# Optimization experiments

Measured on AMD Instinct MI355X. Metric: run time of the kernel, lower is better.

The kernel has to match this reference:

```python
import jax, jax.numpy as jnp
import numpy as np

S, B, N, A, L = 2, 8, 12, 4, 24
C, AUX, EK, K, M, OTH = 256, 16, 64, 256, 8, 32
D2 = C + AUX          # transfromer2 d_model
FF = 2048             # torch TransformerEncoderLayer default dim_feedforward
RIN = 2 * EK + 2 * D2 + 2 * OTH
NLAYERS = 2


def _layernorm(x, g, b, eps=1e-5):
    mu = x.mean(-1, keepdims=True)
    var = ((x - mu) ** 2).mean(-1, keepdims=True)
    return (x - mu) * jax.lax.rsqrt(var + eps) * g + b


def _mha(x, Wq, bq, Wk, bk, Wv, bv, Wo, bo):
    # x: [seq, batch, d]; single head (nhead=1), torch seq-first semantics
    q = x @ Wq.T + bq
    k = x @ Wk.T + bk
    v = x @ Wv.T + bv
    scale = x.shape[-1] ** -0.5
    att = jax.nn.softmax(jnp.einsum('sbd,tbd->bst', q, k) * scale, axis=-1)
    o = jnp.einsum('bst,tbd->sbd', att, v)
    return o @ Wo.T + bo


def _encoder(x, aw, ab, w1, b1, w2, b2, lg, lb):
    # post-norm torch TransformerEncoderLayer, ReLU FFN, dropout off (eval)
    for i in range(aw.shape[0]):
        a = _mha(x, aw[i, 0], ab[i, 0], aw[i, 1], ab[i, 1], aw[i, 2], ab[i, 2], aw[i, 3], ab[i, 3])
        x = _layernorm(x + a, lg[i, 0], lb[i, 0])
        h = jax.nn.relu(x @ w1[i].T + b1[i]) @ w2[i].T + b2[i]
        x = _layernorm(x + h, lg[i, 1], lb[i, 1])
    return x


def _conv(x, w, b, pad):
    y = jax.lax.conv_general_dilated(x, w, (1, 1), [(pad, pad), (0, 0)],
                                     dimension_numbers=('NCHW', 'OIHW', 'NCHW'))
    return y + b[None, :, None, None]


def _forward(chars, att_type, kw_idx, input_idx, static, other,
             char_table, filter_w, filter_b, gate_w, gate_b, mlp_w, mlp_b,
             kw_table, aline_w, aline_b,
             t1_attn_w, t1_attn_b, t1_ffn_w1, t1_ffn_b1, t1_ffn_w2, t1_ffn_b2, t1_ln_g, t1_ln_b,
             t2_attn_w, t2_attn_b, t2_ffn_w1, t2_ffn_b1, t2_ffn_w2, t2_ffn_b2, t2_ln_g, t2_ln_b,
             reg_w1, reg_b1, reg_w2, reg_b2):
    # nn.Embedding(max_norm=1): rows renormalized to norm <= 1
    nrm = jnp.linalg.norm(char_table, axis=1, keepdims=True)
    tbl = char_table * jnp.minimum(1.0, 1.0 / jnp.maximum(nrm, 1e-7))
    ce = tbl[chars]                                  # [S,B,N,A,L,C]
    x = ce.reshape(-1, 1, L, C)                      # strings as conv batch
    f = jnp.tanh(_conv(x, filter_w, filter_b, 1))    # gated conv: tanh * sigmoid
    g = jax.nn.sigmoid(_conv(x, gate_w, gate_b, 1))
    v = _conv(f * g, mlp_w, mlp_b, 0)                # 1x1 conv back to 1 channel
    str_vec = v.reshape(S, B, N, A, L, C).mean(axis=4)   # mean over chars -> [S,B,N,A,C]
    kw_vec = kw_table[kw_idx] @ aline_w.T + aline_b      # keyword path -> [S,B,N,A,C]
    att_vec = jnp.where((att_type == 1)[..., None], kw_vec, str_vec)
    # transfromer1: torch seq-first, seq = nodes, batch = (side, plan, attr)
    x1 = att_vec.transpose(2, 0, 1, 3, 4).reshape(N, S * B * A, C)
    y1 = _encoder(x1, t1_attn_w, t1_attn_b, t1_ffn_w1, t1_ffn_b1, t1_ffn_w2, t1_ffn_b2, t1_ln_g, t1_ln_b)
    node_enc = y1.reshape(N, S, B, A, C).mean(axis=3).transpose(1, 2, 0, 3)  # mean over attrs -> [S,B,N,C]
    h = jnp.concatenate([node_enc, static], axis=-1)                          # [S,B,N,D2]
    # transfromer2: seq = plan batch, batch = (side, node) -- torch seq-first
    x2 = h.transpose(1, 0, 2, 3).reshape(B, S * N, D2)
    y2 = _encoder(x2, t2_attn_w, t2_attn_b, t2_ffn_w1, t2_ffn_b1, t2_ffn_w2, t2_ffn_b2, t2_ln_g, t2_ln_b)
    real = y2.reshape(B, S, N, D2).mean(axis=2)      # mean over nodes -> [B,S,D2]
    inp = kw_table[input_idx].mean(axis=2)           # encoding_input -> [S,B,EK]
    feats = jnp.concatenate([inp[0], real[:, 0], inp[1], real[:, 1], other], axis=1)  # [B,RIN]
    return jax.nn.relu(feats @ reg_w1.T + reg_b1) @ reg_w2.T + reg_b2  # [B,1]


def setup_inputs() -> dict:
    key = jax.random.key(0)
    ks = iter(jax.random.split(key, 64))
    def rn(shape, s=0.02):
        return jax.random.normal(next(ks), shape, jnp.float32) * s
    inp = {
        'chars': jax.random.randint(next(ks), (S, B, N, A, L), 0, 128, jnp.int32),
        'att_type': jax.random.randint(next(ks), (S, B, N, A), 0, 2, jnp.int32),
        'kw_idx': jax.random.randint(next(ks), (S, B, N, A), 0, K, jnp.int32),
        'input_idx': jax.random.randint(next(ks), (S, B, M), 0, K, jnp.int32),
        'static': rn((S, B, N, AUX), 1.0),
        'other': rn((B, 2 * OTH), 1.0),
        'char_table': rn((128, C), 1.0),
        'filter_w': rn((16, 1, 3, 1), 0.2), 'filter_b': rn((16,), 0.02),
        'gate_w': rn((16, 1, 3, 1), 0.2), 'gate_b': rn((16,), 0.02),
        'mlp_w': rn((1, 16, 1, 1), 0.2), 'mlp_b': rn((1,), 0.02),
        'kw_table': rn((K, EK), 0.05),
        'aline_w': rn((C, EK), 0.05), 'aline_b': rn((C,), 0.02),
        't1_attn_w': rn((NLAYERS, 4, C, C), 0.05), 't1_attn_b': rn((NLAYERS, 4, C), 0.02),
        't1_ffn_w1': rn((NLAYERS, FF, C), 0.02), 't1_ffn_b1': rn((NLAYERS, FF), 0.02),
        't1_ffn_w2': rn((NLAYERS, C, FF), 0.02), 't1_ffn_b2': rn((NLAYERS, C), 0.02),
        't1_ln_g': jnp.ones((NLAYERS, 2, C), jnp.float32), 't1_ln_b': jnp.zeros((NLAYERS, 2, C), jnp.float32),
        't2_attn_w': rn((NLAYERS, 4, D2, D2), 0.05), 't2_attn_b': rn((NLAYERS, 4, D2), 0.02),
        't2_ffn_w1': rn((NLAYERS, FF, D2), 0.02), 't2_ffn_b1': rn((NLAYERS, FF), 0.02),
        't2_ffn_w2': rn((NLAYERS, D2, FF), 0.02), 't2_ffn_b2': rn((NLAYERS, D2), 0.02),
        't2_ln_g': jnp.ones((NLAYERS, 2, D2), jnp.float32), 't2_ln_b': jnp.zeros((NLAYERS, 2, D2), jnp.float32),
        'reg_w1': rn((32, RIN), 0.05), 'reg_b1': rn((32,), 0.02),
        'reg_w2': rn((1, 32), 0.1), 'reg_b2': rn((1,), 0.02),
    }
    return inp


def reference(chars, att_type, kw_idx, input_idx, static, other,
              char_table, filter_w, filter_b, gate_w, gate_b, mlp_w, mlp_b,
              kw_table, aline_w, aline_b,
              t1_attn_w, t1_attn_b, t1_ffn_w1, t1_ffn_b1, t1_ffn_w2, t1_ffn_b2, t1_ln_g, t1_ln_b,
              t2_attn_w, t2_attn_b, t2_ffn_w1, t2_ffn_b1, t2_ffn_w2, t2_ffn_b2, t2_ln_g, t2_ln_b,
              reg_w1, reg_b1, reg_w2, reg_b2):
    return _forward(chars, att_type, kw_idx, input_idx, static, other,
                    char_table, filter_w, filter_b, gate_w, gate_b, mlp_w, mlp_b,
                    kw_table, aline_w, aline_b,
                    t1_attn_w, t1_attn_b, t1_ffn_w1, t1_ffn_b1, t1_ffn_w2, t1_ffn_b2, t1_ln_g, t1_ln_b,
                    t2_attn_w, t2_attn_b, t2_ffn_w1, t2_ffn_b1, t2_ffn_w2, t2_ffn_b2, t2_ln_g, t2_ln_b,
                    reg_w1, reg_b1, reg_w2, reg_b2)
```

## Files before the change

kernel.cpp:

```cpp
#include <hip/hip_runtime.h>
#include <math.h>

#define S_ 2
#define B_ 8
#define N_ 12
#define A_ 4
#define L_ 24
#define C_ 256
#define AUX_ 16
#define EK_ 64
#define K_ 256
#define M_ 8
#define OTH_ 32
#define D2_ 272
#define FF_ 2048
#define RIN_ 736
#define NSTR_ (S_*B_*N_*A_)

typedef __attribute__((ext_vector_type(8))) short short8v;
typedef __attribute__((ext_vector_type(4))) float f32x4;

__device__ __forceinline__ unsigned short f2bf(float f) {
    unsigned u = __float_as_uint(f);
    return (unsigned short)((u + 0x7FFFu + ((u >> 16) & 1u)) >> 16);
}

__global__ void cvt_w_k(const float* __restrict__ s0, const float* __restrict__ s1,
                        const float* __restrict__ s2, const float* __restrict__ s3,
                        const float* __restrict__ s4, const float* __restrict__ s5,
                        unsigned short* __restrict__ dst) {
    const int T = 5441536 / 4;
    for (int q = blockIdx.x * 256 + threadIdx.x; q < T; q += gridDim.x * 256) {
        int idx = q * 4;
        const float* src; int off;
        if      (idx < 524288)  { src = s0; off = 0; }
        else if (idx < 1572864) { src = s1; off = 524288; }
        else if (idx < 2621440) { src = s2; off = 1572864; }
        else if (idx < 3213312) { src = s3; off = 2621440; }
        else if (idx < 4327424) { src = s4; off = 3213312; }
        else                    { src = s5; off = 4327424; }
        float4 v = *(const float4*)(src + (idx - off));
        ushort4 o;
        o.x = f2bf(v.x); o.y = f2bf(v.y); o.z = f2bf(v.z); o.w = f2bf(v.w);
        *(ushort4*)(dst + idx) = o;
    }
}

__global__ void scale_table_k(const float* __restrict__ tbl, float* __restrict__ out) {
    int r = blockIdx.x;
    int c = threadIdx.x;
    float v = tbl[r * C_ + c];
    float sq = v * v;
    for (int off = 32; off; off >>= 1) sq += __shfl_down(sq, off);
    __shared__ float red[4];
    __shared__ float scl;
    if ((c & 63) == 0) red[c >> 6] = sq;
    __syncthreads();
    if (c == 0) {
        float n = sqrtf(red[0] + red[1] + red[2] + red[3]);
        scl = fminf(1.f, 1.f / fmaxf(n, 1e-7f));
    }
    __syncthreads();
    out[r * C_ + c] = v * scl;
}

__global__ void attvec_k(const int* __restrict__ chars, const int* __restrict__ att_type,
                         const int* __restrict__ kw_idx, const float* __restrict__ tblS,
                         const float* __restrict__ fw, const float* __restrict__ fb,
                         const float* __restrict__ gw, const float* __restrict__ gb,
                         const float* __restrict__ mw, const float* __restrict__ mb,
                         const float* __restrict__ kwt, const float* __restrict__ aw,
                         const float* __restrict__ ab, float* __restrict__ x1,
                         unsigned short* __restrict__ x1b) {
    int str = blockIdx.x;
    int tid = threadIdx.x;
    int grp = tid >> 8;
    int c = tid & 255;
    __shared__ int ch[L_];
    __shared__ float xv[L_ + 2][C_];
    __shared__ float part[4][C_];
    if (tid < L_) ch[tid] = chars[str * L_ + tid];
    __syncthreads();

    bool kw = (att_type[str] == 1);
    float partial;
    if (kw) {
        const float* kr = kwt + kw_idx[str] * EK_ + grp * 16;
        const float* awr = aw + c * EK_ + grp * 16;
        float acc = (grp == 0) ? ab[c] : 0.f;
        #pragma unroll
        for (int e = 0; e < 16; ++e) acc = fmaf(kr[e], awr[e], acc);
        partial = acc;
    } else {
        #pragma unroll
        for (int i = 0; i < 6; ++i) {
            int l = grp * 6 + i;
            xv[l + 1][c] = tblS[ch[l] * C_ + c];
        }
        if (grp == 0) xv[0][c] = 0.f;
        if (grp == 3) xv[L_ + 1][c] = 0.f;
        __syncthreads();

        float f0[4], f1[4], f2[4], fbv[4], g0[4], g1[4], g2[4], gbv[4], mwv[4];
        #pragma unroll
        for (int oo = 0; oo < 4; ++oo) {
            int o = grp * 4 + oo;
            f0[oo] = 2.f*fw[o*3]; f1[oo] = 2.f*fw[o*3+1]; f2[oo] = 2.f*fw[o*3+2];
            fbv[oo] = 2.f*fb[o];
            g0[oo] = gw[o*3]; g1[oo] = gw[o*3+1]; g2[oo] = gw[o*3+2];
            gbv[oo] = gb[o];
            mwv[oo] = mw[o];
        }
        float osum[4] = {0.f, 0.f, 0.f, 0.f};
        float xm = xv[0][c], x0 = xv[1][c];
        for (int l = 1; l <= L_; ++l) {
            float xp = xv[l + 1][c];
            #pragma unroll
            for (int oo = 0; oo < 4; ++oo) {
                float pf2 = fbv[oo] + f0[oo]*xm + f1[oo]*x0 + f2[oo]*xp;
                float pg  = gbv[oo] + g0[oo]*xm + g1[oo]*x0 + g2[oo]*xp;
                pf2 = fminf(fmaxf(pf2, -30.f), 30.f);
                pg  = fminf(fmaxf(pg,  -15.f), 15.f);
                float e1 = __expf(pf2);
                float e2 = __expf(pg);
                float num = (e1 - 1.f) * e2;
                float den = (e1 + 1.f) * (e2 + 1.f);
                osum[oo] = fmaf(num, __builtin_amdgcn_rcpf(den), osum[oo]);
            }
            xm = x0; x0 = xp;
        }
        partial = mwv[0]*osum[0] + mwv[1]*osum[1] + mwv[2]*osum[2] + mwv[3]*osum[3];
    }
    part[grp][c] = partial;
    __syncthreads();
    if (grp == 0) {
        int a = str & 3;
        int n = (str >> 2) % N_;
        int sb = str / (N_ * A_);
        int row = n * 64 + sb * 4 + a;
        float tot = part[0][c] + part[1][c] + part[2][c] + part[3][c];
        float out = kw ? tot : (mb[0] + tot * (1.f / 24.f));
        x1[row * C_ + c] = out;
        x1b[row * C_ + c] = f2bf(out);
    }
}

__global__ void gemm_mfma_k(const unsigned short* __restrict__ Ab,
                            const unsigned short* __restrict__ Wb,
                            const float* __restrict__ bias, float* __restrict__ Cf,
                            unsigned short* __restrict__ Cb,
                            int R, int K, int N, int relu, int kslice, int obf) {
    int tid = threadIdx.x;
    int wave = tid >> 6, lane = tid & 63;
    int fr = lane & 15, fq = lane >> 4;
    int m0 = blockIdx.y * 64;
    int n0 = blockIdx.x * 64 + wave * 16;
    int kbeg = blockIdx.z * kslice;
    int kend = min(kbeg + kslice, K);
    int col = n0 + fr;
    bool bok = col < N;
    const unsigned short* Wrow = Wb + (size_t)col * K;
    const unsigned short* Ar0 = Ab + (size_t)(m0 + fr) * K;
    const unsigned short* Ar1 = Ab + (size_t)(m0 + 16 + fr) * K;
    const unsigned short* Ar2 = Ab + (size_t)(m0 + 32 + fr) * K;
    const unsigned short* Ar3 = Ab + (size_t)(m0 + 48 + fr) * K;

    f32x4 acc0 = {0.f,0.f,0.f,0.f}, acc1 = {0.f,0.f,0.f,0.f};
    f32x4 acc2 = {0.f,0.f,0.f,0.f}, acc3 = {0.f,0.f,0.f,0.f};
    const short8v z8 = {0,0,0,0,0,0,0,0};

    for (int kt = kbeg; kt < kend; kt += 32) {
        int kl = kt + fq * 8;
        bool kv = (kl + 8 <= kend);
        short8v bf  = (bok && kv) ? *(const short8v*)(Wrow + kl) : z8;
        short8v af0 = kv ? *(const short8v*)(Ar0 + kl) : z8;
        short8v af1 = kv ? *(const short8v*)(Ar1 + kl) : z8;
        short8v af2 = kv ? *(const short8v*)(Ar2 + kl) : z8;
        short8v af3 = kv ? *(const short8v*)(Ar3 + kl) : z8;
        acc0 = __builtin_amdgcn_mfma_f32_16x16x32_bf16(af0, bf, acc0, 0, 0, 0);
        acc1 = __builtin_amdgcn_mfma_f32_16x16x32_bf16(af1, bf, acc1, 0, 0, 0);
        acc2 = __builtin_amdgcn_mfma_f32_16x16x32_bf16(af2, bf, acc2, 0, 0, 0);
        acc3 = __builtin_amdgcn_mfma_f32_16x16x32_bf16(af3, bf, acc3, 0, 0, 0);
    }

    if (!bok) return;
    bool direct = (gridDim.z == 1);
    float bv = direct ? bias[col] : 0.f;
    float* outf = direct ? Cf : (Cf + (size_t)blockIdx.z * R * N);
#define STOREACC(accv, mi) do {                                           \
        _Pragma("unroll")                                                 \
        for (int j = 0; j < 4; ++j) {                                     \
            int row = m0 + (mi)*16 + fq * 4 + j;                          \
            float v = accv[j] + bv;                                       \
            if (direct && relu) v = fmaxf(v, 0.f);                        \
            if (obf) Cb[(size_t)row * N + col] = f2bf(v);                 \
            else     outf[(size_t)row * N + col] = v;                     \
        }                                                                 \
    } while (0)
    STOREACC(acc0, 0); STOREACC(acc1, 1); STOREACC(acc2, 2); STOREACC(acc3, 3);
#undef STOREACC
}

__global__ void attn_k(const float* __restrict__ qkv, unsigned short* __restrict__ ob,
                       int seq, int batch, int d, float scale) {
    __shared__ float sm[3 * 12 * 256];
    __shared__ float sc[12 * 12];
    int j = blockIdx.x, tid = threadIdx.x;
    int sd = seq * d, s3 = 3 * d;
    float* qs = sm;
    float* ks = sm + sd;
    float* vs = sm + 2 * sd;
    for (int idx = tid; idx < sd; idx += 256) {
        int s = idx / d, c = idx - s * d;
        const float* base = qkv + (size_t)(s * batch + j) * s3 + c;
        qs[idx] = base[0];
        ks[idx] = base[d];
        vs[idx] = base[2 * d];
    }
    __syncthreads();
    for (int p = tid; p < seq * seq; p += 256) {
        int s = p / seq, t = p - s * seq;
        float acc = 0.f;
        const float* qp = qs + s * d;
        const float* kp = ks + t * d;
        for (int c = 0; c < d; ++c) acc += qp[c] * kp[c];
        sc[p] = acc * scale;
    }
    __syncthreads();
    if (tid < seq) {
        float m = -1e30f;
        for (int t = 0; t < seq; ++t) m = fmaxf(m, sc[tid * seq + t]);
        float ssum = 0.f;
        for (int t = 0; t < seq; ++t) {
            float e = __expf(sc[tid * seq + t] - m);
            sc[tid * seq + t] = e;
            ssum += e;
        }
        float inv = 1.f / ssum;
        for (int t = 0; t < seq; ++t) sc[tid * seq + t] *= inv;
    }
    __syncthreads();
    for (int c = tid; c < d; c += 256) {
        for (int s = 0; s < seq; ++s) {
            float acc = 0.f;
            for (int t = 0; t < seq; ++t) acc += sc[s * seq + t] * vs[t * d + c];
            ob[(size_t)(s * batch + j) * d + c] = f2bf(acc);
        }
    }
}

__global__ void redln_k(const float* __restrict__ part, const float* __restrict__ bias,
                        float* __restrict__ x, unsigned short* __restrict__ xb,
                        const float* __restrict__ g, const float* __restrict__ b,
                        int d, int NS, int RN) {
    int r = blockIdx.x, tid = threadIdx.x;
    __shared__ float red[10];
    const float* xr = x + (size_t)r * d;
    int i0 = tid, i1 = tid + 256;
    bool h0 = i0 < d, h1 = i1 < d;
    float v0 = 0.f, v1 = 0.f;
    if (h0) {
        v0 = xr[i0] + bias[i0];
        for (int z = 0; z < NS; ++z) v0 += part[(size_t)z * RN + (size_t)r * d + i0];
    }
    if (h1) {
        v1 = xr[i1] + bias[i1];
        for (int z = 0; z < NS; ++z) v1 += part[(size_t)z * RN + (size_t)r * d + i1];
    }
    float s = v0 + v1, ss = v0 * v0 + v1 * v1;
    for (int off = 32; off; off >>= 1) {
        s += __shfl_down(s, off);
        ss += __shfl_down(ss, off);
    }
    if ((tid & 63) == 0) { red[(tid >> 6) * 2] = s; red[(tid >> 6) * 2 + 1] = ss; }
    __syncthreads();
    if (tid == 0) {
        float S = red[0] + red[2] + red[4] + red[6];
        float SS = red[1] + red[3] + red[5] + red[7];
        float mu = S / d;
        float var = SS / d - mu * mu;
        red[8] = mu;
        red[9] = rsqrtf(var + 1e-5f);
    }
    __syncthreads();
    float mu = red[8], inv = red[9];
    float* xw = x + (size_t)r * d;
    if (h0) {
        float o = (v0 - mu) * inv * g[i0] + b[i0];
        xw[i0] = o; xb[(size_t)r * d + i0] = f2bf(o);
    }
    if (h1) {
        float o = (v1 - mu) * inv * g[i1] + b[i1];
        xw[i1] = o; xb[(size_t)r * d + i1] = f2bf(o);
    }
}

__global__ void build_x2_k(const float* __restrict__ y1, const float* __restrict__ stat,
                           float* __restrict__ x2, unsigned short* __restrict__ x2b) {
    int id = blockIdx.x;
    int n = id % N_;
    int b = (id / N_) % B_;
    int s = id / (N_ * B_);
    int orow = b * (S_ * N_) + s * N_ + n;
    for (int c = threadIdx.x; c < D2_; c += 256) {
        float v;
        if (c < C_) {
            int j0 = (s * B_ + b) * A_;
            float acc = 0.f;
            for (int a = 0; a < A_; ++a) acc += y1[(size_t)(n * 64 + j0 + a) * C_ + c];
            v = acc * 0.25f;
        } else {
            v = stat[((size_t)(s * B_ + b) * N_ + n) * AUX_ + (c - C_)];
        }
        x2[(size_t)orow * D2_ + c] = v;
        x2b[(size_t)orow * D2_ + c] = f2bf(v);
    }
}

__global__ void build_real_k(const float* __restrict__ y2, float* __restrict__ real) {
    int id = blockIdx.x;
    int s = id & 1, b = id >> 1;
    for (int c = threadIdx.x; c < D2_; c += 256) {
        float acc = 0.f;
        for (int n = 0; n < N_; ++n) acc += y2[(size_t)(b * 24 + s * N_ + n) * D2_ + c];
        real[(size_t)(b * 2 + s) * D2_ + c] = acc * (1.f / 12.f);
    }
}

__global__ void regressor_k(const float* __restrict__ real, const int* __restrict__ input_idx,
                            const float* __restrict__ kwt, const float* __restrict__ other,
                            const float* __restrict__ w1, const float* __restrict__ b1,
                            const float* __restrict__ w2, const float* __restrict__ b2,
                            float* __restrict__ out) {
    int b = blockIdx.x;
    int tid = threadIdx.x;
    __shared__ float feats[RIN_];
    __shared__ float hh[32];
    for (int i = tid; i < RIN_; i += 256) {
        float v;
        if (i < 64) {
            float acc = 0.f;
            for (int m = 0; m < M_; ++m) acc += kwt[input_idx[b * M_ + m] * EK_ + i];
            v = acc * 0.125f;
        } else if (i < 336) {
            v = real[(size_t)(b * 2 + 0) * D2_ + (i - 64)];
        } else if (i < 400) {
            int e = i - 336;
            float acc = 0.f;
            for (int m = 0; m < M_; ++m) acc += kwt[input_idx[64 + b * M_ + m] * EK_ + e];
            v = acc * 0.125f;
        } else if (i < 672) {
            v = real[(size_t)(b * 2 + 1) * D2_ + (i - 400)];
        } else {
            v = other[b * 64 + (i - 672)];
        }
        feats[i] = v;
    }
    __syncthreads();
    if (tid < 32) {
        float acc = b1[tid];
        const float* wr = w1 + (size_t)tid * RIN_;
        for (int i = 0; i < RIN_; ++i) acc += feats[i] * wr[i];
        hh[tid] = fmaxf(acc, 0.f);
    }
    __syncthreads();
    if (tid == 0) {
        float acc = b2[0];
        for (int j = 0; j < 32; ++j) acc += hh[j] * w2[j];
        out[b] = acc;
    }
}

extern "C" void kernel_launch(void* const* d_in, const int* in_sizes, int n_in,
                              void* d_out, int out_size, void* d_ws, size_t ws_size,
                              hipStream_t stream) {
    const int*   chars      = (const int*)d_in[0];
    const int*   att_type   = (const int*)d_in[1];
    const int*   kw_idx     = (const int*)d_in[2];
    const int*   input_idx  = (const int*)d_in[3];
    const float* stat       = (const float*)d_in[4];
    const float* other      = (const float*)d_in[5];
    const float* char_table = (const float*)d_in[6];
    const float* filter_w   = (const float*)d_in[7];
    const float* filter_b   = (const float*)d_in[8];
    const float* gate_w     = (const float*)d_in[9];
    const float* gate_b     = (const float*)d_in[10];
    const float* mlp_w      = (const float*)d_in[11];
    const float* mlp_b      = (const float*)d_in[12];
    const float* kw_table   = (const float*)d_in[13];
    const float* aline_w    = (const float*)d_in[14];
    const float* aline_b    = (const float*)d_in[15];
    const float* t1_attn_w  = (const float*)d_in[16];
    const float* t1_attn_b  = (const float*)d_in[17];
    const float* t1_ffn_w1  = (const float*)d_in[18];
    const float* t1_ffn_b1  = (const float*)d_in[19];
    const float* t1_ffn_w2  = (const float*)d_in[20];
    const float* t1_ffn_b2  = (const float*)d_in[21];
    const float* t1_ln_g    = (const float*)d_in[22];
    const float* t1_ln_b    = (const float*)d_in[23];
    const float* t2_attn_w  = (const float*)d_in[24];
    const float* t2_attn_b  = (const float*)d_in[25];
    const float* t2_ffn_w1  = (const float*)d_in[26];
    const float* t2_ffn_b1  = (const float*)d_in[27];
    const float* t2_ffn_w2  = (const float*)d_in[28];
    const float* t2_ffn_b2  = (const float*)d_in[29];
    const float* t2_ln_g    = (const float*)d_in[30];
    const float* t2_ln_b    = (const float*)d_in[31];
    const float* reg_w1     = (const float*)d_in[32];
    const float* reg_b1     = (const float*)d_in[33];
    const float* reg_w2     = (const float*)d_in[34];
    const float* reg_b2     = (const float*)d_in[35];

    float* ws   = (float*)d_ws;
    float* tblS = ws;
    float* x1   = tblS + 32768;
    float* qkv  = x1 + 196608;
    float* pbuf = qkv + 589824;
    float* x2   = pbuf + 786432;
    float* realb= x2 + 52224;
    unsigned short* x1b = (unsigned short*)(realb + 4352);
    unsigned short* obb = x1b + 196608;
    unsigned short* hb  = obb + 196608;
    unsigned short* x2b = hb + 1572864;
    unsigned short* wbf = x2b + 52224 + 16;
    unsigned short* wb_t1_attn = wbf;
    unsigned short* wb_t1_ffn1 = wbf + 524288;
    unsigned short* wb_t1_ffn2 = wbf + 1572864;
    unsigned short* wb_t2_attn = wbf + 2621440;
    unsigned short* wb_t2_ffn1 = wbf + 3213312;
    unsigned short* wb_t2_ffn2 = wbf + 4327424;

    auto gemm_f32 = [&](const unsigned short* A, const unsigned short* Wb, const float* bias,
                        float* Cc, int R, int Kk, int N) {
        dim3 g((N + 63) / 64, R / 64, 1);
        gemm_mfma_k<<<g, 256, 0, stream>>>(A, Wb, bias, Cc, (unsigned short*)0,
                                           R, Kk, N, 0, Kk, 0);
    };
    auto gemm_bf16 = [&](const unsigned short* A, const unsigned short* Wb, const float* bias,
                         unsigned short* Cc, int R, int Kk, int N) {
        dim3 g((N + 63) / 64, R / 64, 1);
        gemm_mfma_k<<<g, 256, 0, stream>>>(A, Wb, bias, (float*)0, Cc,
                                           R, Kk, N, 1, Kk, 1);
    };
    auto gemm_split_ln = [&](const unsigned short* A, const unsigned short* Wb,
                             const float* bias, float* x, unsigned short* xb,
                             const float* g, const float* b,
                             int R, int Kk, int N, int ns) {
        int ksl = ((Kk + ns - 1) / ns + 31) / 32 * 32;
        dim3 gr((N + 63) / 64, R / 64, ns);
        gemm_mfma_k<<<gr, 256, 0, stream>>>(A, Wb, bias, pbuf, (unsigned short*)0,
                                            R, Kk, N, 0, ksl, 0);
        redln_k<<<R, 256, 0, stream>>>(pbuf, bias, x, xb, g, b, N, ns, R * N);
    };

    cvt_w_k<<<2048, 256, 0, stream>>>(t1_attn_w, t1_ffn_w1, t1_ffn_w2,
                                      t2_attn_w, t2_ffn_w1, t2_ffn_w2, wbf);
    scale_table_k<<<128, 256, 0, stream>>>(char_table, tblS);
    attvec_k<<<NSTR_, 1024, 0, stream>>>(chars, att_type, kw_idx, tblS,
                                         filter_w, filter_b, gate_w, gate_b,
                                         mlp_w, mlp_b, kw_table, aline_w, aline_b,
                                         x1, x1b);

    for (int i = 0; i < 2; ++i) {
        const unsigned short* awb = wb_t1_attn + (size_t)i * 4 * C_ * C_;
        const float* ab = t1_attn_b + (size_t)i * 4 * C_;
        gemm_f32(x1b, awb, ab, qkv, 768, C_, 3 * C_);
        attn_k<<<64, 256, 0, stream>>>(qkv, obb, 12, 64, C_, 0.0625f);
        gemm_split_ln(obb, awb + 3 * C_ * C_, ab + 3 * C_, x1, x1b,
                      t1_ln_g + i * 2 * C_, t1_ln_b + i * 2 * C_, 768, C_, C_, 2);
        gemm_bf16(x1b, wb_t1_ffn1 + (size_t)i * FF_ * C_, t1_ffn_b1 + i * FF_, hb, 768, C_, FF_);
        gemm_split_ln(hb, wb_t1_ffn2 + (size_t)i * C_ * FF_, t1_ffn_b2 + i * C_, x1, x1b,
                      t1_ln_g + i * 2 * C_ + C_, t1_ln_b + i * 2 * C_ + C_, 768, FF_, C_, 4);
    }

    build_x2_k<<<192, 256, 0, stream>>>(x1, stat, x2, x2b);

    float sc2 = 1.0f / sqrtf(272.0f);
    for (int i = 0; i < 2; ++i) {
        const unsigned short* awb = wb_t2_attn + (size_t)i * 4 * D2_ * D2_;
        const float* ab = t2_attn_b + (size_t)i * 4 * D2_;
        gemm_f32(x2b, awb, ab, qkv, 192, D2_, 3 * D2_);
        attn_k<<<24, 256, 0, stream>>>(qkv, obb, 8, 24, D2_, sc2);
        gemm_split_ln(obb, awb + 3 * D2_ * D2_, ab + 3 * D2_, x2, x2b,
                      t2_ln_g + i * 2 * D2_, t2_ln_b + i * 2 * D2_, 192, D2_, D2_, 4);
        gemm_bf16(x2b, wb_t2_ffn1 + (size_t)i * FF_ * D2_, t2_ffn_b1 + i * FF_, hb, 192, D2_, FF_);
        gemm_split_ln(hb, wb_t2_ffn2 + (size_t)i * D2_ * FF_, t2_ffn_b2 + i * D2_, x2, x2b,
                      t2_ln_g + i * 2 * D2_ + D2_, t2_ln_b + i * 2 * D2_ + D2_, 192, FF_, D2_, 8);
    }

    build_real_k<<<16, 256, 0, stream>>>(x2, realb);
    regressor_k<<<8, 256, 0, stream>>>(realb, input_idx, kw_table, other,
                                       reg_w1, reg_b1, reg_w2, reg_b2, (float*)d_out);
}
```

Baseline: 327.8 us.

## Use persistent atomic work queue for attvec, prefetch GEMM loads, pad attention smem

The string-embedding kernel becomes a persistent grid of 512 blocks that pull strings from an atomic counter, so conv weights are loaded once per block and load imbalance between keyword and conv strings is evened out. Its exponentials switch to exp2 with log2(e) folded into the weights. The MFMA GEMM register-prefetches the next K-slice before issuing the current MFMAs to hide global latency. The attention kernel pads shared rows and splits each score dot product across four lanes with shuffle reductions. The changes add a memset and atomic contention and raise register pressure in the GEMM.

```diff
diff --git a/kernel.cpp b/kernel.cpp
--- a/kernel.cpp
+++ b/kernel.cpp
@@ -71,77 +71,87 @@
                          const float* __restrict__ mw, const float* __restrict__ mb,
                          const float* __restrict__ kwt, const float* __restrict__ aw,
                          const float* __restrict__ ab, float* __restrict__ x1,
-                         unsigned short* __restrict__ x1b) {
-    int str = blockIdx.x;
+                         unsigned short* __restrict__ x1b, int* __restrict__ ctr) {
     int tid = threadIdx.x;
     int grp = tid >> 8;
     int c = tid & 255;
+    __shared__ int su;
     __shared__ int ch[L_];
     __shared__ float xv[L_ + 2][C_];
     __shared__ float part[4][C_];
-    if (tid < L_) ch[tid] = chars[str * L_ + tid];
-    __syncthreads();
-
-    bool kw = (att_type[str] == 1);
-    float partial;
-    if (kw) {
-        const float* kr = kwt + kw_idx[str] * EK_ + grp * 16;
-        const float* awr = aw + c * EK_ + grp * 16;
-        float acc = (grp == 0) ? ab[c] : 0.f;
-        #pragma unroll
-        for (int e = 0; e < 16; ++e) acc = fmaf(kr[e], awr[e], acc);
-        partial = acc;
-    } else {
-        #pragma unroll
-        for (int i = 0; i < 6; ++i) {
-            int l = grp * 6 + i;
-            xv[l + 1][c] = tblS[ch[l] * C_ + c];
+
+    const float L2E = 1.44269504f;
+    float f0[4], f1[4], f2[4], fbv[4], g0[4], g1[4], g2[4], gbv[4], mwv[4];
+    #pragma unroll
+    for (int oo = 0; oo < 4; ++oo) {
+        int o = grp * 4 + oo;
+        f0[oo] = 2.f*L2E*fw[o*3]; f1[oo] = 2.f*L2E*fw[o*3+1]; f2[oo] = 2.f*L2E*fw[o*3+2];
+        fbv[oo] = 2.f*L2E*fb[o];
+        g0[oo] = L2E*gw[o*3]; g1[oo] = L2E*gw[o*3+1]; g2[oo] = L2E*gw[o*3+2];
+        gbv[oo] = L2E*gb[o];
+        mwv[oo] = mw[o];
+    }
+
+    for (;;) {
+        if (tid == 0) su = atomicAdd(ctr, 1);
+        __syncthreads();
+        int str = su;
+        if (str >= NSTR_) break;
+        bool kw = (att_type[str] == 1);
+        float partial;
+        if (kw) {
+            const float* kr = kwt + kw_idx[str] * EK_ + grp * 16;
+            const float* awr = aw + c * EK_ + grp * 16;
+            float acc = (grp == 0) ? ab[c] : 0.f;
+            #pragma unroll
+            for (int e = 0; e < 16; ++e) acc = fmaf(kr[e], awr[e], acc);
+            partial = acc;
+        } else {
+            if (tid < L_) ch[tid] = chars[str * L_ + tid];
+            __syncthreads();
+            #pragma unroll
+            for (int i = 0; i < 6; ++i) {
+                int l = grp * 6 + i;
+                xv[l + 1][c] = tblS[ch[l] * C_ + c];
+            }
+            if (grp == 0) xv[0][c] = 0.f;
+            if (grp == 3) xv[L_ + 1][c] = 0.f;
+            __syncthreads();
+
+            float osum[4] = {0.f, 0.f, 0.f, 0.f};
+            float xm = xv[0][c], x0 = xv[1][c];
+            for (int l = 1; l <= L_; ++l) {
+                float xp = xv[l + 1][c];
+                #pragma unroll
+                for (int oo = 0; oo < 4; ++oo) {
+                    float pf2 = fbv[oo] + f0[oo]*xm + f1[oo]*x0 + f2[oo]*xp;
+                    float pg  = gbv[oo] + g0[oo]*xm + g1[oo]*x0 + g2[oo]*xp;
+                    pf2 = fminf(fmaxf(pf2, -43.f), 43.f);
+                    pg  = fminf(fmaxf(pg,  -22.f), 22.f);
+                    float e1 = __builtin_amdgcn_exp2f(pf2);
+                    float e2 = __builtin_amdgcn_exp2f(pg);
+                    float num = (e1 - 1.f) * e2;
+                    float den = (e1 + 1.f) * (e2 + 1.f);
+                    osum[oo] = fmaf(num, __builtin_amdgcn_rcpf(den), osum[oo]);
+                }
+                xm = x0; x0 = xp;
+            }
+            partial = mwv[0]*osum[0] + mwv[1]*osum[1] + mwv[2]*osum[2] + mwv[3]*osum[3];
+            __syncthreads();
         }
-        if (grp == 0) xv[0][c] = 0.f;
-        if (grp == 3) xv[L_ + 1][c] = 0.f;
+        part[grp][c] = partial;
         __syncthreads();
-
-        float f0[4], f1[4], f2[4], fbv[4], g0[4], g1[4], g2[4], gbv[4], mwv[4];
-        #pragma unroll
-        for (int oo = 0; oo < 4; ++oo) {
-            int o = grp * 4 + oo;
-            f0[oo] = 2.f*fw[o*3]; f1[oo] = 2.f*fw[o*3+1]; f2[oo] = 2.f*fw[o*3+2];
-            fbv[oo] = 2.f*fb[o];
-            g0[oo] = gw[o*3]; g1[oo] = gw[o*3+1]; g2[oo] = gw[o*3+2];
-            gbv[oo] = gb[o];
-            mwv[oo] = mw[o];
+        if (grp == 0) {
+            int a = str & 3;
+            int n = (str >> 2) % N_;
+            int sb = str / (N_ * A_);
+            int row = n * 64 + sb * 4 + a;
+            float tot = part[0][c] + part[1][c] + part[2][c] + part[3][c];
+            float out = kw ? tot : (mb[0] + tot * (1.f / 24.f));
+            x1[row * C_ + c] = out;
+            x1b[row * C_ + c] = f2bf(out);
         }
-        float osum[4] = {0.f, 0.f, 0.f, 0.f};
-        float xm = xv[0][c], x0 = xv[1][c];
-        for (int l = 1; l <= L_; ++l) {
-            float xp = xv[l + 1][c];
-            #pragma unroll
-            for (int oo = 0; oo < 4; ++oo) {
-                float pf2 = fbv[oo] + f0[oo]*xm + f1[oo]*x0 + f2[oo]*xp;
-                float pg  = gbv[oo] + g0[oo]*xm + g1[oo]*x0 + g2[oo]*xp;
-                pf2 = fminf(fmaxf(pf2, -30.f), 30.f);
-                pg  = fminf(fmaxf(pg,  -15.f), 15.f);
-                float e1 = __expf(pf2);
-                float e2 = __expf(pg);
-                float num = (e1 - 1.f) * e2;
-                float den = (e1 + 1.f) * (e2 + 1.f);
-                osum[oo] = fmaf(num, __builtin_amdgcn_rcpf(den), osum[oo]);
-            }
-            xm = x0; x0 = xp;
-        }
-        partial = mwv[0]*osum[0] + mwv[1]*osum[1] + mwv[2]*osum[2] + mwv[3]*osum[3];
-    }
-    part[grp][c] = partial;
-    __syncthreads();
-    if (grp == 0) {
-        int a = str & 3;
-        int n = (str >> 2) % N_;
-        int sb = str / (N_ * A_);
-        int row = n * 64 + sb * 4 + a;
-        float tot = part[0][c] + part[1][c] + part[2][c] + part[3][c];
-        float out = kw ? tot : (mb[0] + tot * (1.f / 24.f));
-        x1[row * C_ + c] = out;
-        x1b[row * C_ + c] = f2bf(out);
+        __syncthreads();
     }
 }
 
@@ -168,20 +178,28 @@
     f32x4 acc0 = {0.f,0.f,0.f,0.f}, acc1 = {0.f,0.f,0.f,0.f};
     f32x4 acc2 = {0.f,0.f,0.f,0.f}, acc3 = {0.f,0.f,0.f,0.f};
     const short8v z8 = {0,0,0,0,0,0,0,0};
-
+    short8v pb, pa0, pa1, pa2, pa3;
+
+#define LDSET(ktv) do {                                                   \
+        int kl2 = (ktv) + fq * 8;                                         \
+        bool kv2 = (kl2 + 8 <= kend);                                     \
+        pb  = (bok && kv2) ? *(const short8v*)(Wrow + kl2) : z8;          \
+        pa0 = kv2 ? *(const short8v*)(Ar0 + kl2) : z8;                    \
+        pa1 = kv2 ? *(const short8v*)(Ar1 + kl2) : z8;                    \
+        pa2 = kv2 ? *(const short8v*)(Ar2 + kl2) : z8;                    \
+        pa3 = kv2 ? *(const short8v*)(Ar3 + kl2) : z8;                    \
+    } while (0)
+
+    LDSET(kbeg);
     for (int kt = kbeg; kt < kend; kt += 32) {
-        int kl = kt + fq * 8;
-        bool kv = (kl + 8 <= kend);
-        short8v bf  = (bok && kv) ? *(const short8v*)(Wrow + kl) : z8;
-        short8v af0 = kv ? *(const short8v*)(Ar0 + kl) : z8;
-        short8v af1 = kv ? *(const short8v*)(Ar1 + kl) : z8;
-        short8v af2 = kv ? *(const short8v*)(Ar2 + kl) : z8;
-        short8v af3 = kv ? *(const short8v*)(Ar3 + kl) : z8;
+        short8v bf = pb, af0 = pa0, af1 = pa1, af2 = pa2, af3 = pa3;
+        if (kt + 32 < kend) LDSET(kt + 32);
         acc0 = __builtin_amdgcn_mfma_f32_16x16x32_bf16(af0, bf, acc0, 0, 0, 0);
         acc1 = __builtin_amdgcn_mfma_f32_16x16x32_bf16(af1, bf, acc1, 0, 0, 0);
         acc2 = __builtin_amdgcn_mfma_f32_16x16x32_bf16(af2, bf, acc2, 0, 0, 0);
         acc3 = __builtin_amdgcn_mfma_f32_16x16x32_bf16(af3, bf, acc3, 0, 0, 0);
     }
+#undef LDSET
 
     if (!bok) return;
     bool direct = (gridDim.z == 1);
@@ -203,28 +221,32 @@
 
 __global__ void attn_k(const float* __restrict__ qkv, unsigned short* __restrict__ ob,
                        int seq, int batch, int d, float scale) {
-    __shared__ float sm[3 * 12 * 256];
+    __shared__ float sm[3 * 12 * 260];
     __shared__ float sc[12 * 12];
     int j = blockIdx.x, tid = threadIdx.x;
-    int sd = seq * d, s3 = 3 * d;
+    int dp = d + 4;
+    int s3 = 3 * d;
     float* qs = sm;
-    float* ks = sm + sd;
-    float* vs = sm + 2 * sd;
-    for (int idx = tid; idx < sd; idx += 256) {
-        int s = idx / d, c = idx - s * d;
-        const float* base = qkv + (size_t)(s * batch + j) * s3 + c;
-        qs[idx] = base[0];
-        ks[idx] = base[d];
-        vs[idx] = base[2 * d];
-    }
-    __syncthreads();
-    for (int p = tid; p < seq * seq; p += 256) {
+    float* ks = sm + 12 * 260;
+    float* vs = sm + 2 * 12 * 260;
+    for (int idx = tid; idx < seq * d; idx += 256) {
+        int s = idx / d, cc = idx - s * d;
+        const float* base = qkv + (size_t)(s * batch + j) * s3 + cc;
+        qs[s * dp + cc] = base[0];
+        ks[s * dp + cc] = base[d];
+        vs[s * dp + cc] = base[2 * d];
+    }
+    __syncthreads();
+    for (int p4 = tid; p4 < seq * seq * 4; p4 += 256) {
+        int p = p4 >> 2, sub = p4 & 3;
         int s = p / seq, t = p - s * seq;
+        const float* qp = qs + s * dp;
+        const float* kp = ks + t * dp;
         float acc = 0.f;
-        const float* qp = qs + s * d;
-        const float* kp = ks + t * d;
-        for (int c = 0; c < d; ++c) acc += qp[c] * kp[c];
-        sc[p] = acc * scale;
+        for (int cc = sub; cc < d; cc += 4) acc = fmaf(qp[cc], kp[cc], acc);
+        acc += __shfl_xor(acc, 1);
+        acc += __shfl_xor(acc, 2);
+        if (sub == 0) sc[p] = acc * scale;
     }
     __syncthreads();
     if (tid < seq) {
@@ -243,7 +265,7 @@
     for (int c = tid; c < d; c += 256) {
         for (int s = 0; s < seq; ++s) {
             float acc = 0.f;
-            for (int t = 0; t < seq; ++t) acc += sc[s * seq + t] * vs[t * d + c];
+            for (int t = 0; t < seq; ++t) acc = fmaf(sc[s * seq + t], vs[t * dp + c], acc);
             ob[(size_t)(s * batch + j) * d + c] = f2bf(acc);
         }
     }
@@ -429,6 +451,7 @@
     unsigned short* wb_t2_attn = wbf + 2621440;
     unsigned short* wb_t2_ffn1 = wbf + 3213312;
     unsigned short* wb_t2_ffn2 = wbf + 4327424;
+    int* ctr = (int*)(wbf + 5441536);
 
     auto gemm_f32 = [&](const unsigned short* A, const unsigned short* Wb, const float* bias,
                         float* Cc, int R, int Kk, int N) {
@@ -453,13 +476,14 @@
         redln_k<<<R, 256, 0, stream>>>(pbuf, bias, x, xb, g, b, N, ns, R * N);
     };
 
+    hipMemsetAsync(ctr, 0, sizeof(int), stream);
     cvt_w_k<<<2048, 256, 0, stream>>>(t1_attn_w, t1_ffn_w1, t1_ffn_w2,
                                       t2_attn_w, t2_ffn_w1, t2_ffn_w2, wbf);
     scale_table_k<<<128, 256, 0, stream>>>(char_table, tblS);
-    attvec_k<<<NSTR_, 1024, 0, stream>>>(chars, att_type, kw_idx, tblS,
-                                         filter_w, filter_b, gate_w, gate_b,
-                                         mlp_w, mlp_b, kw_table, aline_w, aline_b,
-                                         x1, x1b);
+    attvec_k<<<512, 1024, 0, stream>>>(chars, att_type, kw_idx, tblS,
+                                       filter_w, filter_b, gate_w, gate_b,
+                                       mlp_w, mlp_b, kw_table, aline_w, aline_b,
+                                       x1, x1b, ctr);
 
     for (int i = 0; i < 2; ++i) {
         const unsigned short* awb = wb_t1_attn + (size_t)i * 4 * C_ * C_;
```

Result: no change. 326.5 us (-0.4%).
